# Optimization experiments

Hardware: AMD Instinct MI355X
Metric: run time of the kernel (lower is better)

## Reference

```python
import jax, jax.numpy as jnp
import numpy as np

HIDDEN = 4096
N_HEADS = 32
N_KV_HEADS = 8
D_HEAD = HIDDEN // N_HEADS  # 128
SEQ_LEN = 2048
ROPE_THETA = 10000.0


def _rope(t, start_index):
    # t: [L, n_heads, d_head]; rotate-half (Llama-style) RoPE
    L, _, d = t.shape
    inv_freq = 1.0 / (ROPE_THETA ** (jnp.arange(0, d, 2, dtype=jnp.float32) / d))  # [d/2]
    pos = jnp.arange(L, dtype=jnp.float32) + jnp.float32(start_index)  # [L]
    ang = pos[:, None] * inv_freq  # [L, d/2]
    cos = jnp.cos(ang)[:, None, :].astype(t.dtype)  # [L, 1, d/2]
    sin = jnp.sin(ang)[:, None, :].astype(t.dtype)
    t1, t2 = jnp.split(t, 2, axis=-1)
    return jnp.concatenate([t1 * cos - t2 * sin, t1 * sin + t2 * cos], axis=-1)


def setup_inputs() -> dict:
    key = jax.random.key(0)
    ks = jax.random.split(key, 5)
    s = 1.0 / np.sqrt(HIDDEN)
    return {
        "x": jax.random.normal(ks[0], (SEQ_LEN, HIDDEN), dtype=jnp.float32),
        "Wq": jax.random.normal(ks[1], (HIDDEN, N_HEADS * D_HEAD), dtype=jnp.float32) * s,
        "Wk": jax.random.normal(ks[2], (HIDDEN, N_KV_HEADS * D_HEAD), dtype=jnp.float32) * s,
        "Wv": jax.random.normal(ks[3], (HIDDEN, N_KV_HEADS * D_HEAD), dtype=jnp.float32) * s,
        "Wo": jax.random.normal(ks[4], (N_HEADS * D_HEAD, HIDDEN), dtype=jnp.float32) * s,
        "start_index": 0,
    }


def reference(x, Wq, Wk, Wv, Wo, start_index):
    # x: [L, hidden]; start_index==0 -> cache reset, so post-write cache == current k, v
    L, _ = x.shape
    q = (x @ Wq).reshape(L, N_HEADS, D_HEAD)
    k = (x @ Wk).reshape(L, N_KV_HEADS, D_HEAD)
    v = (x @ Wv).reshape(L, N_KV_HEADS, D_HEAD)
    q = _rope(q, start_index)
    k = _rope(k, start_index)
    # KV cache read: full cache is just [L] entries (prefill)
    S = L
    g = N_HEADS // N_KV_HEADS
    qh = q.transpose(1, 0, 2).reshape(N_KV_HEADS, g, L, D_HEAD)  # [kv, g, L, d]
    kh = k.transpose(1, 0, 2)  # [kv, S, d]
    vh = v.transpose(1, 0, 2)  # [kv, S, d]
    scale = 1.0 / np.sqrt(D_HEAD)
    scores = jnp.einsum('kgld,ksd->kgls', qh, kh) * jnp.asarray(scale, qh.dtype)
    # is_causal = (L > 1): tril(L, S) mask
    causal = jnp.tril(jnp.ones((L, S), dtype=bool))
    neg = jnp.asarray(jnp.finfo(scores.dtype).min, scores.dtype)
    scores = jnp.where(causal, scores, neg)
    attn = jax.nn.softmax(scores, axis=-1)
    out = jnp.einsum('kgls,ksd->kgld', attn, vh)  # [kv, g, L, d]
    out = out.reshape(N_HEADS, L, D_HEAD).transpose(1, 0, 2).reshape(L, N_HEADS * D_HEAD)
    return out @ Wo
```

## Files before the change

kernel.cpp:

```cpp
#include <hip/hip_runtime.h>

typedef unsigned short u16;
typedef float f32x4 __attribute__((ext_vector_type(4)));
typedef __bf16 bf16x8 __attribute__((ext_vector_type(8)));
typedef u16 u16x8 __attribute__((ext_vector_type(8)));

#define VMCNT(n) asm volatile("s_waitcnt vmcnt(" #n ")" ::: "memory")

static __device__ __forceinline__ u16 f2bf(float f) {
  union { float f; unsigned u; } v; v.f = f;
  unsigned r = v.u + 0x7fffu + ((v.u >> 16) & 1u);
  return (u16)(r >> 16);
}
static __device__ __forceinline__ float bf2f(u16 x) {
  union { unsigned u; float f; } v; v.u = (unsigned)x << 16; return v.f;
}

static __device__ __forceinline__ f32x4 mfma16(u16x8 a, u16x8 b, f32x4 c) {
  return __builtin_amdgcn_mfma_f32_16x16x32_bf16(
      __builtin_bit_cast(bf16x8, a), __builtin_bit_cast(bf16x8, b), c, 0, 0, 0);
}

static __device__ __forceinline__ void load_lds16(const void* g, void* l) {
  __builtin_amdgcn_global_load_lds(
      (const __attribute__((address_space(1))) void*)g,
      (__attribute__((address_space(3))) void*)l, 16, 0, 0);
}

__global__ void cvt_f32_bf16_swz(const float* __restrict__ in, u16* __restrict__ out, int n8) {
  int i = blockIdx.x * blockDim.x + threadIdx.x;
  if (i >= n8) return;
  int row = i >> 9;
  int j = i & 511;
  int jp = (j & ~7) | ((j & 7) ^ (row & 7));
  const float* src = in + (size_t)i * 8;
  u16x8 o;
  #pragma unroll
  for (int e = 0; e < 8; e++) o[e] = f2bf(src[e]);
  *(u16x8*)(out + ((size_t)row << 12) + jp * 8) = o;
}

__global__ __launch_bounds__(256)
void transpose_cvt(const float* __restrict__ W, u16* __restrict__ Wt, int K, int N) {
  __shared__ float tile[128][33];
  const int k0 = blockIdx.x * 128, n0 = blockIdx.y * 32;
  const int tr = threadIdx.x >> 3;
  const int tc4 = (threadIdx.x & 7) * 4;
  #pragma unroll
  for (int it = 0; it < 4; it++) {
    int kl = it * 32 + tr;
    float4 v = *(const float4*)&W[(size_t)(k0 + kl) * N + n0 + tc4];
    tile[kl][tc4] = v.x; tile[kl][tc4 + 1] = v.y;
    tile[kl][tc4 + 2] = v.z; tile[kl][tc4 + 3] = v.w;
  }
  __syncthreads();
  const int nl = threadIdx.x >> 4;
  const int dch = threadIdx.x & 15;
  #pragma unroll
  for (int it = 0; it < 2; it++) {
    int n = n0 + it * 16 + nl;
    int sch = (dch & 8) | ((dch & 7) ^ (n & 7));
    u16x8 o;
    #pragma unroll
    for (int e = 0; e < 8; e++) o[e] = f2bf(tile[sch * 8 + e][it * 16 + nl]);
    *(u16x8*)&Wt[(size_t)n * K + k0 + dch * 8] = o;
  }
}

__global__ void rope_table_k(float2* __restrict__ tab, const int* __restrict__ start, int L) {
  int i = blockIdx.x * blockDim.x + threadIdx.x;
  if (i >= L * 64) return;
  int p = i >> 6, j = i & 63;
  float inv = powf(10000.0f, -(float)j / 64.0f);
  float ang = (float)(p + start[0]) * inv;
  tab[i] = make_float2(cosf(ang), sinf(ang));
}

__global__ void rope_apply_b(const u16* __restrict__ in, int istride, int icol,
                             u16* __restrict__ outp, const float2* __restrict__ tab,
                             int total, int H, float scale, int swz) {
  int i = blockIdx.x * blockDim.x + threadIdx.x;
  if (i >= total) return;
  int j8 = (i & 7) * 8;
  int h = (i >> 3) % H;
  int p = i / (8 * H);
  const u16* base = in + (size_t)p * istride + icol + h * 128;
  u16x8 a = *(const u16x8*)(base + j8);
  u16x8 b = *(const u16x8*)(base + j8 + 64);
  u16x8 o1, o2;
  #pragma unroll
  for (int e = 0; e < 8; e++) {
    float2 cs = tab[p * 64 + j8 + e];
    float av = bf2f(a[e]), bv = bf2f(b[e]);
    o1[e] = f2bf((av * cs.x - bv * cs.y) * scale);
    o2[e] = f2bf((av * cs.y + bv * cs.x) * scale);
  }
  int c1 = i & 7;
  int cs1 = swz ? (c1 ^ (p & 7)) : c1;
  u16* ob = outp + ((size_t)p * H + h) * 128 + cs1 * 8;
  *(u16x8*)ob = o1;
  *(u16x8*)(ob + 64) = o2;
}

template<int BN, bool OUT_BF16>
__global__ __launch_bounds__(512, 2)
void gemm8p(const u16* __restrict__ A, const u16* __restrict__ Bt,
            float* __restrict__ Cf, u16* __restrict__ Cb, int N, int K, int gm) {
  constexpr int N_REP = BN / 64;
  constexpr int NHALF = N_REP / 2 > 0 ? N_REP / 2 : 1;
  __shared__ alignas(16) u16 As[2][256 * 64];
  __shared__ alignas(16) u16 Bs[2][BN * 64];
  const int tid = threadIdx.x;
  const int lane = tid & 63;
  const int wid = tid >> 6;
  const int ql = lane & 15, kg = lane >> 4;
  const int wr = wid >> 2, wcn = wid & 3;

  const int nb = gridDim.x;
  const int b = blockIdx.x;
  const int swz = (b & 7) * (nb >> 3) + (b >> 3);
  const int m0 = (swz % gm) * 256;
  const int n0 = (swz / gm) * BN;

  const int srow = tid >> 3, schk = tid & 7;
  const u16* abase = A + (size_t)(m0 + srow) * K + schk * 8;
  const u16* bbase = Bt + (size_t)(n0 + srow) * K + schk * 8;

  auto stageA = [&](int buf, int t, int qa) {
    load_lds16(abase + (size_t)(qa * 64) * K + t * 64,
               &As[buf][((qa * 64 + srow) * 8 + schk) * 8]);
  };
  auto stageB = [&](int buf, int t, int rb) {
    load_lds16(bbase + (size_t)(rb * 64) * K + t * 64,
               &Bs[buf][((rb * 64 + srow) * 8 + schk) * 8]);
  };

  f32x4 acc[8][N_REP] = {};
  u16x8 af[4][2];
  u16x8 bfr[2][NHALF][2];
  const int NT = K / 64;

  stageA(0, 0, 0); stageA(0, 0, 2);
  #pragma unroll
  for (int rb = 0; rb < N_REP; rb++) stageB(0, 0, rb);
  stageA(0, 0, 1); stageA(0, 0, 3);
  VMCNT(0);
  __builtin_amdgcn_sched_barrier(0);
  __builtin_amdgcn_s_barrier();

  #pragma unroll 1
  for (int i = 0; i < NT / 2; i++) {
    #pragma unroll
    for (int p = 0; p < 8; p++) {
      const int q = p & 3;
      const int m = q >> 1, n2 = q & 1;
      const int cbuf = (p < 4) ? 0 : 1;
      if (q == 0 || q == 2) {
        #pragma unroll
        for (int mi = 0; mi < 4; mi++)
          #pragma unroll
          for (int kk = 0; kk < 2; kk++) {
            int row = wr * 128 + m * 64 + mi * 16 + ql;
            int ch = ((kk << 2) | kg) ^ (ql & 7);
            af[mi][kk] = *(const u16x8*)&As[cbuf][(row * 8 + ch) * 8];
          }
      }
      if (q == 0 || q == 1) {
        #pragma unroll
        for (int ni = 0; ni < NHALF; ni++)
          #pragma unroll
          for (int kk = 0; kk < 2; kk++) {
            int R = wcn * (16 * N_REP) + n2 * (16 * NHALF) + ni * 16 + ql;
            int ch = ((kk << 2) | kg) ^ (ql & 7);
            bfr[n2][ni][kk] = *(const u16x8*)&Bs[cbuf][(R * 8 + ch) * 8];
          }
      }
      const int st = 2 * i + 1 + (p >= 4 ? 1 : 0);
      const int sbuf = st & 1;
      if (st < NT) {
        if (q == 0) {
          stageA(sbuf, st, 0); stageA(sbuf, st, 2);
          #pragma unroll
          for (int rb = 0; rb < N_REP / 2; rb++) stageB(sbuf, st, rb);
        } else if (q == 1) {
          #pragma unroll
          for (int rb = N_REP / 2; rb < N_REP; rb++) stageB(sbuf, st, rb);
          stageA(sbuf, st, 1); stageA(sbuf, st, 3);
        }
      }
      if (q == 3) VMCNT(0);
      __builtin_amdgcn_sched_barrier(0);
      __builtin_amdgcn_s_barrier();
      asm volatile("s_waitcnt lgkmcnt(0)" ::: "memory");
      __builtin_amdgcn_sched_barrier(0);
      __builtin_amdgcn_s_setprio(1);
      #pragma unroll
      for (int mi = 0; mi < 4; mi++)
        #pragma unroll
        for (int ni = 0; ni < NHALF; ni++)
          #pragma unroll
          for (int kk = 0; kk < 2; kk++)
            acc[m * 4 + mi][n2 * NHALF + ni] =
                mfma16(af[mi][kk], bfr[n2][ni][kk], acc[m * 4 + mi][n2 * NHALF + ni]);
      __builtin_amdgcn_s_setprio(0);
      __builtin_amdgcn_sched_barrier(0);
      __builtin_amdgcn_s_barrier();
    }
  }

  #pragma unroll
  for (int mi = 0; mi < 8; mi++) {
    #pragma unroll
    for (int ni = 0; ni < N_REP; ni++) {
      int row0 = m0 + wr * 128 + mi * 16 + kg * 4;
      int col = n0 + wcn * (16 * N_REP) + ni * 16 + ql;
      #pragma unroll
      for (int r = 0; r < 4; r++) {
        if constexpr (OUT_BF16)
          Cb[(size_t)(row0 + r) * N + col] = f2bf(acc[mi][ni][r]);
        else
          Cf[(size_t)(row0 + r) * N + col] = acc[mi][ni][r];
      }
    }
  }
}

__global__ __launch_bounds__(256, 2)
void attn_k(const u16* __restrict__ qr, const u16* __restrict__ kr,
            const u16* __restrict__ qkv, u16* __restrict__ out) {
  __shared__ alignas(16) u16 Kls[2][64 * 128];
  __shared__ alignas(16) u16 Vt[2][128][72];
  __shared__ alignas(16) u16 Plds[4][16][72];
  const int tid = threadIdx.x;
  const int lane = tid & 63, wave = tid >> 6;
  const int ql = lane & 15, kg = lane >> 4;
  const int h = blockIdx.y, hk = h >> 2;

  const int sl4 = (tid & 15) * 4;
  const int d0s = (tid >> 4) * 8;
  const u16* vbase = qkv + 5120 + (size_t)hk * 128 + d0s;
  const int krow_s = tid >> 4, kcol_s = (tid & 15) * 8;
  const u16* kbase = kr + (size_t)hk * 128 + (size_t)krow_s * 1024 + kcol_s;

  int cur = 0;
  #pragma unroll 1
  for (int half_idx = 0; half_idx < 2; half_idx++) {
    const int tile = half_idx ? (31 - (int)blockIdx.x) : (int)blockIdx.x;
    const int q0 = tile * 64;
    const int qw = q0 + wave * 16;
    const int nsteps = tile + 1;

    u16x8 qf[4];
    const u16* qbase = qr + ((size_t)(qw + ql) * 32 + h) * 128;
    #pragma unroll
    for (int kk = 0; kk < 4; kk++)
      qf[kk] = *(const u16x8*)(qbase + kk * 32 + kg * 8);

    f32x4 acc[8] = {};
    float m_run = -3e38f, l_run = 0.f;

    __syncthreads();
    cur = 0;
    #pragma unroll
    for (int r = 0; r < 4; r++)
      load_lds16(kbase + (size_t)r * 16 * 1024, &Kls[0][(r * 256 + tid) * 8]);
    u16x8 vreg[4];
    #pragma unroll
    for (int j = 0; j < 4; j++)
      vreg[j] = *(const u16x8*)(vbase + (size_t)(sl4 + j) * 6144);

    #pragma unroll 1
    for (int t = 0; t < nsteps; t++) {
      const int s0 = t * 64;
      #pragma unroll
      for (int e = 0; e < 8; e++) {
        ushort4 w;
        w.x = vreg[0][e]; w.y = vreg[1][e]; w.z = vreg[2][e]; w.w = vreg[3][e];
        *(ushort4*)&Vt[cur][d0s + e][sl4] = w;
      }
      __syncthreads();
      if (t + 1 < nsteps) {
        const u16* kn = kbase + (size_t)(s0 + 64) * 1024;
        #pragma unroll
        for (int r = 0; r < 4; r++)
          load_lds16(kn + (size_t)r * 16 * 1024, &Kls[cur ^ 1][(r * 256 + tid) * 8]);
        #pragma unroll
        for (int j = 0; j < 4; j++)
          vreg[j] = *(const u16x8*)(vbase + (size_t)(s0 + 64 + sl4 + j) * 6144);
      }
      f32x4 sc[4] = {};
      __builtin_amdgcn_s_setprio(1);
      #pragma unroll
      for (int sb = 0; sb < 4; sb++) {
        const u16* krow = &Kls[cur][(sb * 16 + ql) * 128];
        #pragma unroll
        for (int kk = 0; kk < 4; kk++) {
          u16x8 kf = *(const u16x8*)(krow + (((kk * 4 + kg) ^ (ql & 7)) * 8));
          sc[sb] = mfma16(kf, qf[kk], sc[sb]);
        }
      }
      __builtin_amdgcn_s_setprio(0);
      const int qg = qw + ql;
      float mt = -3e38f;
      #pragma unroll
      for (int sb = 0; sb < 4; sb++)
        #pragma unroll
        for (int r = 0; r < 4; r++) {
          int s = s0 + sb * 16 + kg * 4 + r;
          float v = (s > qg) ? -3e38f : sc[sb][r];
          sc[sb][r] = v;
          mt = fmaxf(mt, v);
        }
      mt = fmaxf(mt, __shfl_xor(mt, 16, 64));
      mt = fmaxf(mt, __shfl_xor(mt, 32, 64));
      if (!__all(mt - m_run <= 11.5f)) {
        float m_new = fmaxf(m_run, mt);
        float fco = exp2f(m_run - m_new);
        float fr[4];
        #pragma unroll
        for (int r = 0; r < 4; r++) fr[r] = __shfl(fco, (lane & 48) | (kg * 4 + r), 64);
        #pragma unroll
        for (int db = 0; db < 8; db++)
          #pragma unroll
          for (int r = 0; r < 4; r++) acc[db][r] *= fr[r];
        l_run *= fco;
        m_run = m_new;
      }
      float rs = 0.f;
      #pragma unroll
      for (int sb = 0; sb < 4; sb++)
        #pragma unroll
        for (int r = 0; r < 4; r++) {
          float e = exp2f(sc[sb][r] - m_run);
          sc[sb][r] = e;
          rs += e;
        }
      rs += __shfl_xor(rs, 16, 64);
      rs += __shfl_xor(rs, 32, 64);
      l_run += rs;
      #pragma unroll
      for (int sb = 0; sb < 4; sb++) {
        ushort4 pk;
        pk.x = f2bf(sc[sb][0]); pk.y = f2bf(sc[sb][1]);
        pk.z = f2bf(sc[sb][2]); pk.w = f2bf(sc[sb][3]);
        *(ushort4*)&Plds[wave][ql][sb * 16 + kg * 4] = pk;
      }
      __builtin_amdgcn_s_setprio(1);
      #pragma unroll
      for (int hf = 0; hf < 2; hf++) {
        u16x8 pf = *(const u16x8*)&Plds[wave][ql][hf * 32 + kg * 8];
        #pragma unroll
        for (int db = 0; db < 8; db++) {
          u16x8 vf = *(const u16x8*)&Vt[cur][db * 16 + ql][hf * 32 + kg * 8];
          acc[db] = mfma16(pf, vf, acc[db]);
        }
      }
      __builtin_amdgcn_s_setprio(0);
      cur ^= 1;
    }

    float linv[4];
    #pragma unroll
    for (int r = 0; r < 4; r++)
      linv[r] = 1.f / __shfl(l_run, (lane & 48) | (kg * 4 + r), 64);
    #pragma unroll
    for (int db = 0; db < 8; db++) {
      int d = db * 16 + ql;
      #pragma unroll
      for (int r = 0; r < 4; r++) {
        int q = qw + kg * 4 + r;
        int col = (h * 128 + d) ^ ((q & 7) << 3);
        out[(size_t)q * 4096 + col] = f2bf(acc[db][r] * linv[r]);
      }
    }
  }
}

extern "C" void kernel_launch(void* const* d_in, const int* in_sizes, int n_in,
                              void* d_out, int out_size, void* d_ws, size_t ws_size,
                              hipStream_t stream) {
  const float* x  = (const float*)d_in[0];
  const float* Wq = (const float*)d_in[1];
  const float* Wk = (const float*)d_in[2];
  const float* Wv = (const float*)d_in[3];
  const float* Wo = (const float*)d_in[4];
  const int* start = (const int*)d_in[5];

  const int L = 2048, HID = 4096, NH = 32, NKV = 8;
  const int NQ = 4096, NKVD = 1024, NF = 6144;

  char* ws = (char*)d_ws;
  size_t off = 0;
  auto alloc = [&](size_t bytes) {
    void* p = ws + off;
    off += (bytes + 255) & ~(size_t)255;
    return p;
  };
  u16* x_b   = (u16*)alloc((size_t)L * HID * 2);
  u16* Wq_t  = (u16*)alloc((size_t)NQ * HID * 2);
  u16* Wk_t  = (u16*)alloc((size_t)NKVD * HID * 2);
  u16* Wv_t  = (u16*)alloc((size_t)NKVD * HID * 2);
  u16* Wo_t  = (u16*)alloc((size_t)HID * NQ * 2);
  u16* q_r   = (u16*)alloc((size_t)L * NQ * 2);
  u16* k_r   = (u16*)alloc((size_t)L * NKVD * 2);
  float2* tab = (float2*)alloc((size_t)L * 64 * sizeof(float2));
  u16* qkv_b  = (u16*)d_out;
  u16* attn_b = Wq_t;

  const float qscale = 0.08838834764831845f * 1.4426950408889634f;

  cvt_f32_bf16_swz<<<(L * HID / 8 + 255) / 256, 256, 0, stream>>>(x, x_b, L * HID / 8);
  transpose_cvt<<<dim3(HID / 128, NQ / 32), 256, 0, stream>>>(Wq, Wq_t, HID, NQ);
  transpose_cvt<<<dim3(HID / 128, NKVD / 32), 256, 0, stream>>>(Wk, Wk_t, HID, NKVD);
  transpose_cvt<<<dim3(HID / 128, NKVD / 32), 256, 0, stream>>>(Wv, Wv_t, HID, NKVD);
  transpose_cvt<<<dim3(NQ / 128, HID / 32), 256, 0, stream>>>(Wo, Wo_t, NQ, HID);
  rope_table_k<<<(L * 64 + 255) / 256, 256, 0, stream>>>(tab, start, L);

  gemm8p<256, true><<<192, 512, 0, stream>>>(x_b, Wq_t, nullptr, qkv_b, NF, HID, 8);

  rope_apply_b<<<(L * NH * 8 + 255) / 256, 256, 0, stream>>>(qkv_b, NF, 0, q_r, tab, L * NH * 8, NH, qscale, 0);
  rope_apply_b<<<(L * NKV * 8 + 255) / 256, 256, 0, stream>>>(qkv_b, NF, NQ, k_r, tab, L * NKV * 8, NKV, 1.0f, 1);

  attn_k<<<dim3(16, NH), 256, 0, stream>>>(q_r, k_r, qkv_b, attn_b);

  gemm8p<128, false><<<256, 512, 0, stream>>>(attn_b, Wo_t, (float*)d_out, nullptr, HID, NQ, 8);
}
```

Measured before the change: 376.4 us.

## Reschedule GEMM LDS prefetch to issue A tiles earlier with partial vmcnt waits

Reorders the global-to-LDS staging in the double-buffered GEMM main loop. The first half of the next-next A tile is now prefetched ahead of time, and loads are spread across more phases. The full vmcnt(0) drain at each half-iteration becomes vmcnt(2), except in the tail. The goal is to keep more loads in flight and hide memory latency, but it depends on exact vmcnt accounting and on buffer reuse timing being race-free.

Result: faster. 366.6 us (-2.6%).

```diff
diff --git a/kernel.cpp b/kernel.cpp
--- a/kernel.cpp
+++ b/kernel.cpp
@@ -126,13 +126,19 @@
   const u16* abase = A + (size_t)(m0 + srow) * K + schk * 8;
   const u16* bbase = Bt + (size_t)(n0 + srow) * K + schk * 8;
 
-  auto stageA = [&](int buf, int t, int qa) {
-    load_lds16(abase + (size_t)(qa * 64) * K + t * 64,
-               &As[buf][((qa * 64 + srow) * 8 + schk) * 8]);
+  auto stageA = [&](int buf, int t, int half) {
+    #pragma unroll
+    for (int r = 0; r < 2; r++) {
+      int reg = half * 2 + r;
+      load_lds16(abase + (size_t)(reg * 64) * K + t * 64,
+                 &As[buf][((reg * 64 + srow) * 8 + schk) * 8]);
+    }
   };
-  auto stageB = [&](int buf, int t, int rb) {
-    load_lds16(bbase + (size_t)(rb * 64) * K + t * 64,
-               &Bs[buf][((rb * 64 + srow) * 8 + schk) * 8]);
+  auto stageB = [&](int buf, int t) {
+    #pragma unroll
+    for (int rb = 0; rb < N_REP; rb++)
+      load_lds16(bbase + (size_t)(rb * 64) * K + t * 64,
+                 &Bs[buf][((rb * 64 + srow) * 8 + schk) * 8]);
   };
 
   f32x4 acc[8][N_REP] = {};
@@ -140,16 +146,16 @@
   u16x8 bfr[2][NHALF][2];
   const int NT = K / 64;
 
-  stageA(0, 0, 0); stageA(0, 0, 2);
-  #pragma unroll
-  for (int rb = 0; rb < N_REP; rb++) stageB(0, 0, rb);
-  stageA(0, 0, 1); stageA(0, 0, 3);
+  stageA(0, 0, 0); stageA(0, 0, 1); stageB(0, 0);
+  stageA(1, 1, 0);
   VMCNT(0);
   __builtin_amdgcn_sched_barrier(0);
   __builtin_amdgcn_s_barrier();
 
   #pragma unroll 1
   for (int i = 0; i < NT / 2; i++) {
+    const bool tail = (i == NT / 2 - 1);
+    const int t1 = 2 * i + 1, t2 = 2 * i + 2, t3 = 2 * i + 3;
     #pragma unroll
     for (int p = 0; p < 8; p++) {
       const int q = p & 3;
@@ -175,20 +181,15 @@
             bfr[n2][ni][kk] = *(const u16x8*)&Bs[cbuf][(R * 8 + ch) * 8];
           }
       }
-      const int st = 2 * i + 1 + (p >= 4 ? 1 : 0);
-      const int sbuf = st & 1;
-      if (st < NT) {
-        if (q == 0) {
-          stageA(sbuf, st, 0); stageA(sbuf, st, 2);
-          #pragma unroll
-          for (int rb = 0; rb < N_REP / 2; rb++) stageB(sbuf, st, rb);
-        } else if (q == 1) {
-          #pragma unroll
-          for (int rb = N_REP / 2; rb < N_REP; rb++) stageB(sbuf, st, rb);
-          stageA(sbuf, st, 1); stageA(sbuf, st, 3);
-        }
-      }
-      if (q == 3) VMCNT(0);
+      if (p == 0)      stageA(1, t1, 1);
+      else if (p == 1) stageB(1, t1);
+      else if (p == 2) { if (t2 < NT) stageA(0, t2, 0); }
+      else if (p == 4) { if (t2 < NT) stageA(0, t2, 1); }
+      else if (p == 5) { if (t2 < NT) stageB(0, t2); }
+      else if (p == 6) { if (t3 < NT) stageA(1, t3, 0); }
+      if (p == 3 || p == 7) {
+        if (tail) VMCNT(0); else VMCNT(2);
+      }
       __builtin_amdgcn_sched_barrier(0);
       __builtin_amdgcn_s_barrier();
       asm volatile("s_waitcnt lgkmcnt(0)" ::: "memory");
```

## Shrink GEMM tiles to 128-row blocks with finer-grained vmcnt pipelining

Applied to the files above, without the earlier changes.

Reworks the GEMM kernel from 512-thread 256xBN tiles to 256-thread 128xBN tiles (BN=192 for QKV, 128 for output projection), doubling the grid to 512 blocks for better CU occupancy and tail balance. Global-to-LDS staging is spread across all four phases with partial vmcnt waits instead of a full drain every other phase, aiming to overlap loads with MFMA. In exchange, smaller tiles mean less operand reuse per block and more global traffic, and the hand-tuned vmcnt counts are fragile.

Result: faster. 325.3 us (-13.6%).

```diff
diff --git a/kernel.cpp b/kernel.cpp
--- a/kernel.cpp
+++ b/kernel.cpp
@@ -103,53 +103,53 @@
 }
 
 template<int BN, bool OUT_BF16>
-__global__ __launch_bounds__(512, 2)
+__global__ __launch_bounds__(256, 2)
 void gemm8p(const u16* __restrict__ A, const u16* __restrict__ Bt,
             float* __restrict__ Cf, u16* __restrict__ Cb, int N, int K, int gm) {
-  constexpr int N_REP = BN / 64;
-  constexpr int NHALF = N_REP / 2 > 0 ? N_REP / 2 : 1;
-  __shared__ alignas(16) u16 As[2][256 * 64];
+  constexpr int N_REP = BN / 32;
+  constexpr int NHALF = N_REP / 2;
+  __shared__ alignas(16) u16 As[2][128 * 64];
   __shared__ alignas(16) u16 Bs[2][BN * 64];
   const int tid = threadIdx.x;
   const int lane = tid & 63;
   const int wid = tid >> 6;
   const int ql = lane & 15, kg = lane >> 4;
-  const int wr = wid >> 2, wcn = wid & 3;
+  const int wr = wid >> 1, wcn = wid & 1;
 
   const int nb = gridDim.x;
   const int b = blockIdx.x;
   const int swz = (b & 7) * (nb >> 3) + (b >> 3);
-  const int m0 = (swz % gm) * 256;
+  const int m0 = (swz % gm) * 128;
   const int n0 = (swz / gm) * BN;
 
   const int srow = tid >> 3, schk = tid & 7;
   const u16* abase = A + (size_t)(m0 + srow) * K + schk * 8;
   const u16* bbase = Bt + (size_t)(n0 + srow) * K + schk * 8;
 
-  auto stageA = [&](int buf, int t, int qa) {
-    load_lds16(abase + (size_t)(qa * 64) * K + t * 64,
-               &As[buf][((qa * 64 + srow) * 8 + schk) * 8]);
+  auto stA = [&](int buf, int t, int c) {
+    load_lds16(abase + (size_t)(c * 32) * K + t * 64,
+               &As[buf][((c * 32 + srow) * 8 + schk) * 8]);
   };
-  auto stageB = [&](int buf, int t, int rb) {
-    load_lds16(bbase + (size_t)(rb * 64) * K + t * 64,
-               &Bs[buf][((rb * 64 + srow) * 8 + schk) * 8]);
+  auto stB = [&](int buf, int t, int c) {
+    load_lds16(bbase + (size_t)(c * 32) * K + t * 64,
+               &Bs[buf][((c * 32 + srow) * 8 + schk) * 8]);
   };
 
-  f32x4 acc[8][N_REP] = {};
-  u16x8 af[4][2];
+  f32x4 acc[4][N_REP] = {};
+  u16x8 af[2][2];
   u16x8 bfr[2][NHALF][2];
   const int NT = K / 64;
 
-  stageA(0, 0, 0); stageA(0, 0, 2);
-  #pragma unroll
-  for (int rb = 0; rb < N_REP; rb++) stageB(0, 0, rb);
-  stageA(0, 0, 1); stageA(0, 0, 3);
+  stA(0, 0, 0); stA(0, 0, 1); stA(0, 0, 2); stA(0, 0, 3);
+  #pragma unroll
+  for (int c = 0; c < BN / 32; c++) stB(0, 0, c);
   VMCNT(0);
   __builtin_amdgcn_sched_barrier(0);
   __builtin_amdgcn_s_barrier();
 
   #pragma unroll 1
   for (int i = 0; i < NT / 2; i++) {
+    const bool tail = (i == NT / 2 - 1);
     #pragma unroll
     for (int p = 0; p < 8; p++) {
       const int q = p & 3;
@@ -157,10 +157,10 @@
       const int cbuf = (p < 4) ? 0 : 1;
       if (q == 0 || q == 2) {
         #pragma unroll
-        for (int mi = 0; mi < 4; mi++)
+        for (int mi = 0; mi < 2; mi++)
           #pragma unroll
           for (int kk = 0; kk < 2; kk++) {
-            int row = wr * 128 + m * 64 + mi * 16 + ql;
+            int row = wr * 64 + m * 32 + mi * 16 + ql;
             int ch = ((kk << 2) | kg) ^ (ql & 7);
             af[mi][kk] = *(const u16x8*)&As[cbuf][(row * 8 + ch) * 8];
           }
@@ -178,30 +178,44 @@
       const int st = 2 * i + 1 + (p >= 4 ? 1 : 0);
       const int sbuf = st & 1;
       if (st < NT) {
-        if (q == 0) {
-          stageA(sbuf, st, 0); stageA(sbuf, st, 2);
-          #pragma unroll
-          for (int rb = 0; rb < N_REP / 2; rb++) stageB(sbuf, st, rb);
-        } else if (q == 1) {
-          #pragma unroll
-          for (int rb = N_REP / 2; rb < N_REP; rb++) stageB(sbuf, st, rb);
-          stageA(sbuf, st, 1); stageA(sbuf, st, 3);
-        }
-      }
-      if (q == 3) VMCNT(0);
+        if constexpr (BN == 192) {
+          if (q == 0) { stA(sbuf, st, 0); stA(sbuf, st, 2); stB(sbuf, st, 0); }
+          else if (q == 1) { stB(sbuf, st, 1); stB(sbuf, st, 3); stB(sbuf, st, 4); }
+          else if (q == 2) { stB(sbuf, st, 2); stB(sbuf, st, 5); }
+          else { stA(sbuf, st, 1); stA(sbuf, st, 3); }
+        } else {
+          if (q == 0) { stA(sbuf, st, 0); stA(sbuf, st, 2); stB(sbuf, st, 0); }
+          else if (q == 1) { stB(sbuf, st, 2); stB(sbuf, st, 1); }
+          else if (q == 2) { stB(sbuf, st, 3); }
+          else { stA(sbuf, st, 1); stA(sbuf, st, 3); }
+        }
+      }
+      if (!tail || p < 4) {
+        if constexpr (BN == 192) {
+          if (q == 1) VMCNT(6);
+          else if (q == 3) VMCNT(4);
+          else VMCNT(5);
+        } else {
+          if (q == 0 || q == 1) VMCNT(5);
+          else VMCNT(3);
+        }
+      } else {
+        if (p == 4) VMCNT(2);
+        else VMCNT(0);
+      }
       __builtin_amdgcn_sched_barrier(0);
       __builtin_amdgcn_s_barrier();
       asm volatile("s_waitcnt lgkmcnt(0)" ::: "memory");
       __builtin_amdgcn_sched_barrier(0);
       __builtin_amdgcn_s_setprio(1);
       #pragma unroll
-      for (int mi = 0; mi < 4; mi++)
+      for (int mi = 0; mi < 2; mi++)
         #pragma unroll
         for (int ni = 0; ni < NHALF; ni++)
           #pragma unroll
           for (int kk = 0; kk < 2; kk++)
-            acc[m * 4 + mi][n2 * NHALF + ni] =
-                mfma16(af[mi][kk], bfr[n2][ni][kk], acc[m * 4 + mi][n2 * NHALF + ni]);
+            acc[m * 2 + mi][n2 * NHALF + ni] =
+                mfma16(af[mi][kk], bfr[n2][ni][kk], acc[m * 2 + mi][n2 * NHALF + ni]);
       __builtin_amdgcn_s_setprio(0);
       __builtin_amdgcn_sched_barrier(0);
       __builtin_amdgcn_s_barrier();
@@ -209,17 +223,17 @@
   }
 
   #pragma unroll
-  for (int mi = 0; mi < 8; mi++) {
-    #pragma unroll
-    for (int ni = 0; ni < N_REP; ni++) {
-      int row0 = m0 + wr * 128 + mi * 16 + kg * 4;
-      int col = n0 + wcn * (16 * N_REP) + ni * 16 + ql;
+  for (int a = 0; a < 4; a++) {
+    #pragma unroll
+    for (int j = 0; j < N_REP; j++) {
+      int row0 = m0 + wr * 64 + (a >> 1) * 32 + (a & 1) * 16 + kg * 4;
+      int col = n0 + wcn * (16 * N_REP) + j * 16 + ql;
       #pragma unroll
       for (int r = 0; r < 4; r++) {
         if constexpr (OUT_BF16)
-          Cb[(size_t)(row0 + r) * N + col] = f2bf(acc[mi][ni][r]);
+          Cb[(size_t)(row0 + r) * N + col] = f2bf(acc[a][j][r]);
         else
-          Cf[(size_t)(row0 + r) * N + col] = acc[mi][ni][r];
+          Cf[(size_t)(row0 + r) * N + col] = acc[a][j][r];
       }
     }
   }
@@ -416,12 +430,12 @@
   transpose_cvt<<<dim3(NQ / 128, HID / 32), 256, 0, stream>>>(Wo, Wo_t, NQ, HID);
   rope_table_k<<<(L * 64 + 255) / 256, 256, 0, stream>>>(tab, start, L);
 
-  gemm8p<256, true><<<192, 512, 0, stream>>>(x_b, Wq_t, nullptr, qkv_b, NF, HID, 8);
+  gemm8p<192, true><<<512, 256, 0, stream>>>(x_b, Wq_t, nullptr, qkv_b, NF, HID, 16);
 
   rope_apply_b<<<(L * NH * 8 + 255) / 256, 256, 0, stream>>>(qkv_b, NF, 0, q_r, tab, L * NH * 8, NH, qscale, 0);
   rope_apply_b<<<(L * NKV * 8 + 255) / 256, 256, 0, stream>>>(qkv_b, NF, NQ, k_r, tab, L * NKV * 8, NKV, 1.0f, 1);
 
   attn_k<<<dim3(16, NH), 256, 0, stream>>>(q_r, k_r, qkv_b, attn_b);
 
-  gemm8p<128, false><<<256, 512, 0, stream>>>(attn_b, Wo_t, (float*)d_out, nullptr, HID, NQ, 8);
-}
+  gemm8p<128, false><<<512, 256, 0, stream>>>(attn_b, Wo_t, (float*)d_out, nullptr, HID, NQ, 16);
+}
```
